# Kernel optimization log

Measured on AMD Instinct MI355X. Metric: run time of the kernel, lower is better.

The kernel has to match this reference:

```python
import jax, jax.numpy as jnp
import numpy as np

K = 32
EPS = 1e-16


def setup_inputs() -> dict:
    key = jax.random.key(0)
    k1, k2, k3 = jax.random.split(key, 3)
    N_l, N_h, D, F = 8192, 32768, 3, 128
    x = jax.random.normal(k1, (N_l, F), dtype=jnp.float32)
    pos_l = jax.random.normal(k2, (N_l, D), dtype=jnp.float32)
    pos_h = jax.random.normal(k3, (N_h, D), dtype=jnp.float32)
    return {"x": x, "pos_l": pos_l, "pos_h": pos_h}


def reference(x, pos_l, pos_h):
    # Squared pairwise distances [N_h, N_l] via ||h||^2 - 2 h.l + ||l||^2
    h2 = jnp.sum(pos_h * pos_h, axis=1, keepdims=True)        # [N_h, 1]
    l2 = jnp.sum(pos_l * pos_l, axis=1)                        # [N_l]
    d2 = h2 - 2.0 * (pos_h @ pos_l.T) + l2[None, :]            # [N_h, N_l]
    # k nearest source points per target point
    neg_d2k, idx = jax.lax.top_k(-d2, K)                       # [N_h, K]
    d2k = -neg_d2k
    # Inverse squared-distance weights (torch_geometric: 1/clamp(d2, min=1e-16))
    w = 1.0 / jnp.maximum(d2k, EPS)                            # [N_h, K]
    xk = x[idx]                                                # [N_h, K, F]
    y = jnp.einsum('nk,nkf->nf', w, xk) / jnp.sum(w, axis=1, keepdims=True)
    return y
```

## Files before the change

### kernel.cpp

```cpp
#include <hip/hip_runtime.h>
#include <stdint.h>

#define NL     8192
#define NH     32768
#define FDIM   128
#define KSEL   32
#define CHUNK  1024
#define NCHUNK (NL / CHUNK)
#define QPW    8
#define NWAVES 4
#define BLOCK  (NWAVES * 64)
#define QPB    (NWAVES * QPW)
#define BUFCAP 128

__device__ __forceinline__ int imin(int a, int b) { return a < b ? a : b; }
__device__ __forceinline__ int imax(int a, int b) { return a > b ? a : b; }

__global__ __launch_bounds__(BLOCK, 4)
void knn_interp_kernel(const float* __restrict__ x,
                       const float* __restrict__ pos_l,
                       const float* __restrict__ pos_h,
                       float* __restrict__ out)
{
    __shared__ float4   s_cand[CHUNK];
    __shared__ uint16_t s_idx[QPB][BUFCAP];
    __shared__ uint32_t s_cnt[QPB];
    __shared__ float    s_wd2[QPB][KSEL];
    __shared__ uint16_t s_widx[QPB][KSEL];

    const int tid   = threadIdx.x;
    const int lane  = tid & 63;
    const int wid   = tid >> 6;
    const int qbase = blockIdx.x * QPB + wid * QPW;

    float hx2[QPW], hy2[QPW], hz2[QPW], h2c[QPW];
#pragma unroll
    for (int q = 0; q < QPW; ++q) {
        const float ax = pos_h[(qbase + q) * 3 + 0];
        const float ay = pos_h[(qbase + q) * 3 + 1];
        const float az = pos_h[(qbase + q) * 3 + 2];
        hx2[q] = -2.0f * ax; hy2[q] = -2.0f * ay; hz2[q] = -2.0f * az;
        h2c[q] = ax * ax + ay * ay + az * az;
    }

    float rmin[QPW];
#pragma unroll
    for (int q = 0; q < QPW; ++q) rmin[q] = INFINITY;

    for (int c = 0; c < NCHUNK; ++c) {
        __syncthreads();
        for (int i = tid; i < CHUNK; i += BLOCK) {
            const int g = c * CHUNK + i;
            const float px = pos_l[g * 3 + 0];
            const float py = pos_l[g * 3 + 1];
            const float pz = pos_l[g * 3 + 2];
            s_cand[i] = make_float4(px, py, pz, px * px + py * py + pz * pz);
        }
        __syncthreads();
#pragma unroll 4
        for (int i = 0; i < CHUNK / 64; ++i) {
            const float4 p = s_cand[i * 64 + lane];
#pragma unroll
            for (int q = 0; q < QPW; ++q) {
                float d2 = fmaf(hx2[q], p.x, p.w);
                d2 = fmaf(hy2[q], p.y, d2);
                d2 = fmaf(hz2[q], p.z, d2);
                d2 = d2 + h2c[q];
                rmin[q] = fminf(rmin[q], d2);
            }
        }
    }

    float tau_acc[QPW];
#pragma unroll
    for (int q = 0; q < QPW; ++q) {
        float v = rmin[q];
#pragma unroll
        for (int k = 2; k <= 64; k <<= 1) {
#pragma unroll
            for (int j = k >> 1; j >= 1; j >>= 1) {
                const float o     = __shfl_xor(v, j);
                const bool  up    = ((lane & k) == 0);
                const bool  lower = ((lane & j) == 0);
                v = (lower == up) ? fminf(v, o) : fmaxf(v, o);
            }
        }
        const float tau = __shfl(v, 31);
        tau_acc[q] = tau + 1e-4f;
    }

    if (tid < QPB) s_cnt[tid] = 0;

    for (int c = 0; c < NCHUNK; ++c) {
        __syncthreads();
        for (int i = tid; i < CHUNK; i += BLOCK) {
            const int g = c * CHUNK + i;
            const float px = pos_l[g * 3 + 0];
            const float py = pos_l[g * 3 + 1];
            const float pz = pos_l[g * 3 + 2];
            s_cand[i] = make_float4(px, py, pz, px * px + py * py + pz * pz);
        }
        __syncthreads();
#pragma unroll 2
        for (int i = 0; i < CHUNK / 64; ++i) {
            const int ci = i * 64 + lane;
            const float4 p = s_cand[ci];
#pragma unroll
            for (int q = 0; q < QPW; ++q) {
                float d2 = fmaf(hx2[q], p.x, p.w);
                d2 = fmaf(hy2[q], p.y, d2);
                d2 = fmaf(hz2[q], p.z, d2);
                d2 = d2 + h2c[q];
                if (d2 <= tau_acc[q]) {
                    const uint32_t pos = atomicAdd(&s_cnt[wid * QPW + q], 1u);
                    if (pos < BUFCAP) s_idx[wid * QPW + q][pos] = (uint16_t)(c * CHUNK + ci);
                }
            }
        }
    }

#pragma unroll 1
    for (int q = 0; q < QPW; ++q) {
        const int qq = wid * QPW + q;
        uint32_t M = s_cnt[qq];
        if (M > BUFCAP) M = BUFCAP;

        const double axd = (double)(-0.5f * hx2[q]);
        const double ayd = (double)(-0.5f * hy2[q]);
        const double azd = (double)(-0.5f * hz2[q]);

        const int i0 = ((uint32_t)(2 * lane)     < M) ? (int)s_idx[qq][2 * lane]     : -1;
        const int i1 = ((uint32_t)(2 * lane + 1) < M) ? (int)s_idx[qq][2 * lane + 1] : -1;
        float f0 = INFINITY, f1 = INFINITY;
        if (i0 >= 0) {
            const double dx = (double)pos_l[i0 * 3 + 0] - axd;
            const double dy = (double)pos_l[i0 * 3 + 1] - ayd;
            const double dz = (double)pos_l[i0 * 3 + 2] - azd;
            f0 = (float)(dx * dx + dy * dy + dz * dz);
        }
        if (i1 >= 0) {
            const double dx = (double)pos_l[i1 * 3 + 0] - axd;
            const double dy = (double)pos_l[i1 * 3 + 1] - ayd;
            const double dz = (double)pos_l[i1 * 3 + 2] - azd;
            f1 = (float)(dx * dx + dy * dy + dz * dz);
        }

        int v0 = __float_as_int(f0);
        int v1 = __float_as_int(f1);
#pragma unroll
        for (int k = 2; k <= 128; k <<= 1) {
            const bool up = ((lane & (k >> 1)) == 0);
#pragma unroll
            for (int j = k >> 1; j >= 2; j >>= 1) {
                const int  xo    = j >> 1;
                const bool lower = ((lane & xo) == 0);
                const int o0 = __shfl_xor(v0, xo);
                const int o1 = __shfl_xor(v1, xo);
                v0 = (lower == up) ? imin(v0, o0) : imax(v0, o0);
                v1 = (lower == up) ? imin(v1, o1) : imax(v1, o1);
            }
            const int mn = imin(v0, v1), mx = imax(v0, v1);
            v0 = up ? mn : mx;
            v1 = up ? mx : mn;
        }
        const int tau32 = __shfl(v1, 15);

        const bool a0 = (i0 >= 0) && (__float_as_int(f0) <= tau32);
        const bool a1 = (i1 >= 0) && (__float_as_int(f1) <= tau32);
        const unsigned long long b0 = __ballot(a0);
        const unsigned long long b1 = __ballot(a1);
        const unsigned long long mb = (lane == 63) ? 0x7FFFFFFFFFFFFFFFull
                                                   : ((1ull << (lane + 1)) - 1ull) >> 1;
        const int base = __popcll(b0 & mb) + __popcll(b1 & mb);
        const int p0 = base;
        const int p1 = base + (a0 ? 1 : 0);
        if (a0 && p0 < KSEL) { s_wd2[qq][p0] = f0; s_widx[qq][p0] = (uint16_t)i0; }
        if (a1 && p1 < KSEL) { s_wd2[qq][p1] = f1; s_widx[qq][p1] = (uint16_t)i1; }
    }

#pragma unroll 1
    for (int q = 0; q < QPW; ++q) {
        const int qq = wid * QPW + q;
        const int gq = qbase + q;
        float acc0 = 0.0f, acc1 = 0.0f, wsum = 0.0f;
#pragma unroll 8
        for (int kk = 0; kk < KSEL; ++kk) {
            const float d2  = s_wd2[qq][kk];
            const float w   = 1.0f / fmaxf(d2, 1e-16f);
            const int   idx = (int)s_widx[qq][kk];
            const float* row = x + (size_t)idx * FDIM;
            acc0 = fmaf(w, row[lane], acc0);
            acc1 = fmaf(w, row[lane + 64], acc1);
            wsum += w;
        }
        const float invw = 1.0f / wsum;
        out[(size_t)gq * FDIM + lane]      = acc0 * invw;
        out[(size_t)gq * FDIM + 64 + lane] = acc1 * invw;
    }
}

extern "C" void kernel_launch(void* const* d_in, const int* in_sizes, int n_in,
                              void* d_out, int out_size, void* d_ws, size_t ws_size,
                              hipStream_t stream) {
    const float* x     = (const float*)d_in[0];
    const float* pos_l = (const float*)d_in[1];
    const float* pos_h = (const float*)d_in[2];
    float* out = (float*)d_out;
    dim3 grid(NH / QPB);
    dim3 block(BLOCK);
    hipLaunchKernelGGL(knn_interp_kernel, grid, block, 0, stream,
                       x, pos_l, pos_h, out);
}
```

Measured before the change: 193.4 us.

## Use packed FP32 FMA with SoA pair layout for distance scans

Stores each candidate chunk as structure-of-arrays float2 pairs (x, y, z, squared norm) and evaluates distances for two candidates against two queries using inline v_pk_fma_f32 asm. The |h|^2 constant is dropped from the scan distances, so the per-query threshold and selection now work on d2 - |h|^2, which leaves ordering unchanged. This is meant to halve VALU work in both distance-scan passes. The final gather uses float2 loads and stores plus the hardware rcp instruction, which trades a little reciprocal precision for fewer instructions.

```diff
diff --git a/kernel.cpp b/kernel.cpp
--- a/kernel.cpp
+++ b/kernel.cpp
@@ -13,8 +13,23 @@
 #define QPB    (NWAVES * QPW)
 #define BUFCAP 128
 
+typedef float f32x2 __attribute__((ext_vector_type(2)));
+
 __device__ __forceinline__ int imin(int a, int b) { return a < b ? a : b; }
 __device__ __forceinline__ int imax(int a, int b) { return a > b ? a : b; }
+
+__device__ __forceinline__ f32x2 pk_fma_lo(f32x2 s0, f32x2 s1, f32x2 s2) {
+    f32x2 d;
+    asm("v_pk_fma_f32 %0, %1, %2, %3 op_sel:[0,0,0] op_sel_hi:[1,0,1]"
+        : "=v"(d) : "v"(s0), "v"(s1), "v"(s2));
+    return d;
+}
+__device__ __forceinline__ f32x2 pk_fma_hi(f32x2 s0, f32x2 s1, f32x2 s2) {
+    f32x2 d;
+    asm("v_pk_fma_f32 %0, %1, %2, %3 op_sel:[0,1,0] op_sel_hi:[1,1,1]"
+        : "=v"(d) : "v"(s0), "v"(s1), "v"(s2));
+    return d;
+}
 
 __global__ __launch_bounds__(BLOCK, 4)
 void knn_interp_kernel(const float* __restrict__ x,
@@ -22,7 +37,7 @@
                        const float* __restrict__ pos_h,
                        float* __restrict__ out)
 {
-    __shared__ float4   s_cand[CHUNK];
+    __shared__ f32x2    s_x[CHUNK/2], s_y[CHUNK/2], s_z[CHUNK/2], s_w[CHUNK/2];
     __shared__ uint16_t s_idx[QPB][BUFCAP];
     __shared__ uint32_t s_cnt[QPB];
     __shared__ float    s_wd2[QPB][KSEL];
@@ -33,87 +48,120 @@
     const int wid   = tid >> 6;
     const int qbase = blockIdx.x * QPB + wid * QPW;
 
-    float hx2[QPW], hy2[QPW], hz2[QPW], h2c[QPW];
+    f32x2 hxq[QPW/2], hyq[QPW/2], hzq[QPW/2];
+#pragma unroll
+    for (int j = 0; j < QPW/2; ++j) {
+        const float a0x = pos_h[(size_t)(qbase + 2*j    ) * 3 + 0];
+        const float a0y = pos_h[(size_t)(qbase + 2*j    ) * 3 + 1];
+        const float a0z = pos_h[(size_t)(qbase + 2*j    ) * 3 + 2];
+        const float a1x = pos_h[(size_t)(qbase + 2*j + 1) * 3 + 0];
+        const float a1y = pos_h[(size_t)(qbase + 2*j + 1) * 3 + 1];
+        const float a1z = pos_h[(size_t)(qbase + 2*j + 1) * 3 + 2];
+        hxq[j] = (f32x2){-2.0f * a0x, -2.0f * a1x};
+        hyq[j] = (f32x2){-2.0f * a0y, -2.0f * a1y};
+        hzq[j] = (f32x2){-2.0f * a0z, -2.0f * a1z};
+    }
+
+    f32x2 rminp[QPW];
+#pragma unroll
+    for (int q = 0; q < QPW; ++q) rminp[q] = (f32x2){INFINITY, INFINITY};
+
+    for (int c = 0; c < NCHUNK; ++c) {
+        __syncthreads();
+        for (int i = tid; i < CHUNK/2; i += BLOCK) {
+            const float* p = pos_l + (size_t)(c * CHUNK + 2 * i) * 3;
+            const f32x2 A = *(const f32x2*)(p + 0);
+            const f32x2 B = *(const f32x2*)(p + 2);
+            const f32x2 C = *(const f32x2*)(p + 4);
+            s_x[i] = (f32x2){A.x, B.y};
+            s_y[i] = (f32x2){A.y, C.x};
+            s_z[i] = (f32x2){B.x, C.y};
+            s_w[i] = (f32x2){fmaf(A.x, A.x, fmaf(A.y, A.y, B.x * B.x)),
+                             fmaf(B.y, B.y, fmaf(C.x, C.x, C.y * C.y))};
+        }
+        __syncthreads();
+#pragma unroll
+        for (int i = 0; i < CHUNK/128; ++i) {
+            const int pi = i * 64 + lane;
+            const f32x2 xp = s_x[pi], yp = s_y[pi], zp = s_z[pi], wp = s_w[pi];
+#pragma unroll
+            for (int j = 0; j < QPW/2; ++j) {
+                f32x2 t0 = pk_fma_lo(xp, hxq[j], wp);
+                t0 = pk_fma_lo(yp, hyq[j], t0);
+                t0 = pk_fma_lo(zp, hzq[j], t0);
+                rminp[2*j].x = fminf(rminp[2*j].x, t0.x);
+                rminp[2*j].y = fminf(rminp[2*j].y, t0.y);
+                f32x2 t1 = pk_fma_hi(xp, hxq[j], wp);
+                t1 = pk_fma_hi(yp, hyq[j], t1);
+                t1 = pk_fma_hi(zp, hzq[j], t1);
+                rminp[2*j+1].x = fminf(rminp[2*j+1].x, t1.x);
+                rminp[2*j+1].y = fminf(rminp[2*j+1].y, t1.y);
+            }
+        }
+    }
+
+    float tau_acc[QPW];
 #pragma unroll
     for (int q = 0; q < QPW; ++q) {
-        const float ax = pos_h[(qbase + q) * 3 + 0];
-        const float ay = pos_h[(qbase + q) * 3 + 1];
-        const float az = pos_h[(qbase + q) * 3 + 2];
-        hx2[q] = -2.0f * ax; hy2[q] = -2.0f * ay; hz2[q] = -2.0f * az;
-        h2c[q] = ax * ax + ay * ay + az * az;
-    }
-
-    float rmin[QPW];
-#pragma unroll
-    for (int q = 0; q < QPW; ++q) rmin[q] = INFINITY;
+        float v = fminf(rminp[q].x, rminp[q].y);
+#pragma unroll
+        for (int k = 2; k <= 64; k <<= 1) {
+#pragma unroll
+            for (int jj = k >> 1; jj >= 1; jj >>= 1) {
+                const float o     = __shfl_xor(v, jj);
+                const bool  up    = ((lane & k) == 0);
+                const bool  lower = ((lane & jj) == 0);
+                v = (lower == up) ? fminf(v, o) : fmaxf(v, o);
+            }
+        }
+        tau_acc[q] = __shfl(v, 31) + 1e-4f;
+    }
+
+    if (tid < QPB) s_cnt[tid] = 0;
 
     for (int c = 0; c < NCHUNK; ++c) {
         __syncthreads();
-        for (int i = tid; i < CHUNK; i += BLOCK) {
-            const int g = c * CHUNK + i;
-            const float px = pos_l[g * 3 + 0];
-            const float py = pos_l[g * 3 + 1];
-            const float pz = pos_l[g * 3 + 2];
-            s_cand[i] = make_float4(px, py, pz, px * px + py * py + pz * pz);
-        }
-        __syncthreads();
-#pragma unroll 4
-        for (int i = 0; i < CHUNK / 64; ++i) {
-            const float4 p = s_cand[i * 64 + lane];
-#pragma unroll
-            for (int q = 0; q < QPW; ++q) {
-                float d2 = fmaf(hx2[q], p.x, p.w);
-                d2 = fmaf(hy2[q], p.y, d2);
-                d2 = fmaf(hz2[q], p.z, d2);
-                d2 = d2 + h2c[q];
-                rmin[q] = fminf(rmin[q], d2);
-            }
-        }
-    }
-
-    float tau_acc[QPW];
-#pragma unroll
-    for (int q = 0; q < QPW; ++q) {
-        float v = rmin[q];
-#pragma unroll
-        for (int k = 2; k <= 64; k <<= 1) {
-#pragma unroll
-            for (int j = k >> 1; j >= 1; j >>= 1) {
-                const float o     = __shfl_xor(v, j);
-                const bool  up    = ((lane & k) == 0);
-                const bool  lower = ((lane & j) == 0);
-                v = (lower == up) ? fminf(v, o) : fmaxf(v, o);
-            }
-        }
-        const float tau = __shfl(v, 31);
-        tau_acc[q] = tau + 1e-4f;
-    }
-
-    if (tid < QPB) s_cnt[tid] = 0;
-
-    for (int c = 0; c < NCHUNK; ++c) {
-        __syncthreads();
-        for (int i = tid; i < CHUNK; i += BLOCK) {
-            const int g = c * CHUNK + i;
-            const float px = pos_l[g * 3 + 0];
-            const float py = pos_l[g * 3 + 1];
-            const float pz = pos_l[g * 3 + 2];
-            s_cand[i] = make_float4(px, py, pz, px * px + py * py + pz * pz);
+        for (int i = tid; i < CHUNK/2; i += BLOCK) {
+            const float* p = pos_l + (size_t)(c * CHUNK + 2 * i) * 3;
+            const f32x2 A = *(const f32x2*)(p + 0);
+            const f32x2 B = *(const f32x2*)(p + 2);
+            const f32x2 C = *(const f32x2*)(p + 4);
+            s_x[i] = (f32x2){A.x, B.y};
+            s_y[i] = (f32x2){A.y, C.x};
+            s_z[i] = (f32x2){B.x, C.y};
+            s_w[i] = (f32x2){fmaf(A.x, A.x, fmaf(A.y, A.y, B.x * B.x)),
+                             fmaf(B.y, B.y, fmaf(C.x, C.x, C.y * C.y))};
         }
         __syncthreads();
 #pragma unroll 2
-        for (int i = 0; i < CHUNK / 64; ++i) {
-            const int ci = i * 64 + lane;
-            const float4 p = s_cand[ci];
-#pragma unroll
-            for (int q = 0; q < QPW; ++q) {
-                float d2 = fmaf(hx2[q], p.x, p.w);
-                d2 = fmaf(hy2[q], p.y, d2);
-                d2 = fmaf(hz2[q], p.z, d2);
-                d2 = d2 + h2c[q];
-                if (d2 <= tau_acc[q]) {
-                    const uint32_t pos = atomicAdd(&s_cnt[wid * QPW + q], 1u);
-                    if (pos < BUFCAP) s_idx[wid * QPW + q][pos] = (uint16_t)(c * CHUNK + ci);
+        for (int i = 0; i < CHUNK/128; ++i) {
+            const int pi = i * 64 + lane;
+            const f32x2 xp = s_x[pi], yp = s_y[pi], zp = s_z[pi], wp = s_w[pi];
+            const int g0 = c * CHUNK + 2 * pi;
+#pragma unroll
+            for (int j = 0; j < QPW/2; ++j) {
+                f32x2 t0 = pk_fma_lo(xp, hxq[j], wp);
+                t0 = pk_fma_lo(yp, hyq[j], t0);
+                t0 = pk_fma_lo(zp, hzq[j], t0);
+                f32x2 t1 = pk_fma_hi(xp, hxq[j], wp);
+                t1 = pk_fma_hi(yp, hyq[j], t1);
+                t1 = pk_fma_hi(zp, hzq[j], t1);
+                const int q0 = wid * QPW + 2*j;
+                if (t0.x <= tau_acc[2*j]) {
+                    const uint32_t p0 = atomicAdd(&s_cnt[q0], 1u);
+                    if (p0 < BUFCAP) s_idx[q0][p0] = (uint16_t)g0;
+                }
+                if (t0.y <= tau_acc[2*j]) {
+                    const uint32_t p0 = atomicAdd(&s_cnt[q0], 1u);
+                    if (p0 < BUFCAP) s_idx[q0][p0] = (uint16_t)(g0 + 1);
+                }
+                if (t1.x <= tau_acc[2*j+1]) {
+                    const uint32_t p0 = atomicAdd(&s_cnt[q0 + 1], 1u);
+                    if (p0 < BUFCAP) s_idx[q0 + 1][p0] = (uint16_t)g0;
+                }
+                if (t1.y <= tau_acc[2*j+1]) {
+                    const uint32_t p0 = atomicAdd(&s_cnt[q0 + 1], 1u);
+                    if (p0 < BUFCAP) s_idx[q0 + 1][p0] = (uint16_t)(g0 + 1);
                 }
             }
         }
@@ -125,9 +173,9 @@
         uint32_t M = s_cnt[qq];
         if (M > BUFCAP) M = BUFCAP;
 
-        const double axd = (double)(-0.5f * hx2[q]);
-        const double ayd = (double)(-0.5f * hy2[q]);
-        const double azd = (double)(-0.5f * hz2[q]);
+        const double axd = (double)pos_h[(size_t)(qbase + q) * 3 + 0];
+        const double ayd = (double)pos_h[(size_t)(qbase + q) * 3 + 1];
+        const double azd = (double)pos_h[(size_t)(qbase + q) * 3 + 2];
 
         const int i0 = ((uint32_t)(2 * lane)     < M) ? (int)s_idx[qq][2 * lane]     : -1;
         const int i1 = ((uint32_t)(2 * lane + 1) < M) ? (int)s_idx[qq][2 * lane + 1] : -1;
@@ -182,20 +230,20 @@
     for (int q = 0; q < QPW; ++q) {
         const int qq = wid * QPW + q;
         const int gq = qbase + q;
-        float acc0 = 0.0f, acc1 = 0.0f, wsum = 0.0f;
+        f32x2 acc = (f32x2){0.0f, 0.0f};
+        float wsum = 0.0f;
 #pragma unroll 8
         for (int kk = 0; kk < KSEL; ++kk) {
-            const float d2  = s_wd2[qq][kk];
-            const float w   = 1.0f / fmaxf(d2, 1e-16f);
-            const int   idx = (int)s_widx[qq][kk];
-            const float* row = x + (size_t)idx * FDIM;
-            acc0 = fmaf(w, row[lane], acc0);
-            acc1 = fmaf(w, row[lane + 64], acc1);
+            const float d2 = s_wd2[qq][kk];
+            const float w  = __builtin_amdgcn_rcpf(fmaxf(d2, 1e-16f));
+            const int  idx = (int)s_widx[qq][kk];
+            const f32x2 r2 = *(const f32x2*)(x + (size_t)idx * FDIM + 2 * lane);
+            acc.x = fmaf(w, r2.x, acc.x);
+            acc.y = fmaf(w, r2.y, acc.y);
             wsum += w;
         }
-        const float invw = 1.0f / wsum;
-        out[(size_t)gq * FDIM + lane]      = acc0 * invw;
-        out[(size_t)gq * FDIM + 64 + lane] = acc1 * invw;
+        const float invw = __builtin_amdgcn_rcpf(wsum);
+        *(f32x2*)(out + (size_t)gq * FDIM + 2 * lane) = (f32x2){acc.x * invw, acc.y * invw};
     }
 }
 
```

Result: faster. 182.2 us (-5.8%).
